# Performance work log

Measured on AMD Instinct MI355X. Metric: run time of the kernel, lower is better.

The kernel has to match this reference:

```python
import jax, jax.numpy as jnp
import numpy as np

B, T, C = 4, 2048, 1024
N_HEAD = 16
HEAD_DIM = C // N_HEAD

def setup_inputs() -> dict:
    key = jax.random.key(0)
    k1, k2, k3 = jax.random.split(key, 3)
    x = jax.random.normal(k1, (B, T, C), dtype=jnp.float32)
    # nn.Linear(C, 3C, bias=False): weight [3C, C], y = x @ W.T
    w_qkv = jax.random.normal(k2, (3 * C, C), dtype=jnp.float32) * (1.0 / np.sqrt(C))
    w_proj = jax.random.normal(k3, (C, C), dtype=jnp.float32) * (1.0 / np.sqrt(C))
    return {"x": x, "w_qkv": w_qkv, "w_proj": w_proj}

def reference(x, w_qkv, w_proj):
    Bx, Tx, Cx = x.shape
    qkv = x @ w_qkv.T  # [B,T,3C]
    q, k, v = jnp.split(qkv, 3, axis=-1)
    def heads(t):
        return t.reshape(Bx, Tx, N_HEAD, HEAD_DIM).transpose(0, 2, 1, 3)  # [B,H,T,D]
    q, k, v = heads(q), heads(k), heads(v)
    scale = HEAD_DIM ** -0.5
    att = jnp.einsum('bhtd,bhsd->bhts', q, k) * scale  # [B,H,T,T]
    causal = jnp.tril(jnp.ones((Tx, Tx), dtype=bool))
    att = jnp.where(causal[None, None], att, -jnp.inf)
    att = jax.nn.softmax(att, axis=-1)
    y = jnp.einsum('bhts,bhsd->bhtd', att, v)  # [B,H,T,D]
    y = y.transpose(0, 2, 1, 3).reshape(Bx, Tx, Cx)
    return y @ w_proj.T
```

## Files before the change

kernel.cpp:

```cpp
#include <hip/hip_runtime.h>
#include <hip/hip_bf16.h>

typedef __attribute__((ext_vector_type(8))) short bf16x8;
typedef __attribute__((ext_vector_type(4))) float f32x4;
typedef __attribute__((ext_vector_type(4))) unsigned short ushort4v;
typedef __attribute__((ext_vector_type(2))) unsigned uint2v;

__device__ __forceinline__ unsigned short f2bf(float f) {
  union { float f; unsigned u; } v; v.f = f;
  unsigned r = v.u + 0x7FFFu + ((v.u >> 16) & 1u);
  return (unsigned short)(r >> 16);
}

__device__ __forceinline__ unsigned pack_bf2(float lo, float hi) {
  __hip_bfloat162 h = __float22bfloat162_rn(make_float2(lo, hi));
  union { __hip_bfloat162 h; unsigned u; } cv; cv.h = h; return cv.u;
}

__device__ __forceinline__ void gll16(const void* g, void* l) {
  __builtin_amdgcn_global_load_lds((const __attribute__((address_space(1))) void*)g,
                                   (__attribute__((address_space(3))) void*)l, 16, 0, 0);
}

#define MFMA16(a, b, c) __builtin_amdgcn_mfma_f32_16x16x32_bf16((a), (b), (c), 0, 0, 0)

__global__ void cvt_f32_bf16(const float* __restrict__ s, unsigned short* __restrict__ d, int n) {
  int i = (blockIdx.x * blockDim.x + threadIdx.x) * 4;
  if (i >= n) return;
  float4 f = *(const float4*)(s + i);
  ushort4v r;
  r[0] = f2bf(f.x); r[1] = f2bf(f.y); r[2] = f2bf(f.z); r[3] = f2bf(f.w);
  *(ushort4v*)(d + i) = r;
}

template<int EPI, int MIF>
__global__ __launch_bounds__(512, 1)
void gemm4p(const unsigned short* __restrict__ A,
            const unsigned short* __restrict__ B,
            unsigned short* __restrict__ obf,
            float* __restrict__ of32,
            int M, int N, int K) {
  extern __shared__ unsigned short lds[];
  constexpr int BM = MIF * 32;
  constexpr int ABUF = BM * 32;
  constexpr int BBASE = 3 * ABUF;
  const int tid = threadIdx.x, wid = tid >> 6, lane = tid & 63;
  const int c = lane & 15, g = lane >> 4;
  const int wm = wid >> 2, wn = wid & 3;
  const int nbn = N >> 8;
  const int nwg = gridDim.x;
  int wg = (blockIdx.x & 7) * (nwg >> 3) + (blockIdx.x >> 3);
  const int m0 = (wg / nbn) * BM, n0 = (wg % nbn) * 256;
  const int NT = K >> 5;
  const size_t rb = (size_t)K * 2;
  const int swz = (c & 3) << 4;

  const int r16 = lane >> 2;
  const int sl = (lane & 3) ^ (r16 & 3);
  const char* Ag = (const char*)A + (size_t)(m0 + r16) * rb + sl * 16;
  const char* Bg = (const char*)B + (size_t)(n0 + r16) * rb + sl * 16;

  auto stageA = [&](int t, int buf) {
#pragma unroll
    for (int j = 0; j < MIF / 4; ++j) {
      int ch = wid * (MIF / 4) + j;
      gll16(Ag + (size_t)(ch * 16) * rb + t * 64, lds + buf * ABUF + ch * 512);
    }
  };
  auto stageB = [&](int t, int buf) {
#pragma unroll
    for (int j = 0; j < 2; ++j) {
      int ch = wid * 2 + j;
      gll16(Bg + (size_t)(ch * 16) * rb + t * 64, lds + BBASE + buf * 8192 + ch * 512);
    }
  };

  f32x4 acc[MIF][4];
#pragma unroll
  for (int i = 0; i < MIF; ++i)
#pragma unroll
    for (int j = 0; j < 4; ++j) acc[i][j] = f32x4{0.f, 0.f, 0.f, 0.f};

  stageA(0, 0); stageB(0, 0); stageA(1, 1); stageB(1, 1);
  if constexpr (MIF == 8) { asm volatile("s_waitcnt vmcnt(4)" ::: "memory"); }
  else                    { asm volatile("s_waitcnt vmcnt(3)" ::: "memory"); }
  __builtin_amdgcn_s_barrier();

  for (int t = 0; t < NT; ++t) {
    const int cur = t % 3;
    const unsigned short* Ac = lds + cur * ABUF;
    const unsigned short* Bc = lds + BBASE + cur * 8192;
    const bool more = (t + 2 < NT);
    const int nbuf = (t + 2) % 3;
    bf16x8 af[MIF], bfr[4];
#pragma unroll
    for (int mi = 0; mi < MIF / 2; ++mi) {
      int arow = wm * (MIF * 16) + mi * 16 + c;
      af[mi] = *(const bf16x8*)((const char*)Ac + arow * 64 + ((g * 16) ^ swz));
    }
#pragma unroll
    for (int ni = 0; ni < 4; ++ni) {
      int brow = wn * 64 + ni * 16 + c;
      bfr[ni] = *(const bf16x8*)((const char*)Bc + brow * 64 + ((g * 16) ^ swz));
    }
    if (more) stageA(t + 2, nbuf);
    __builtin_amdgcn_s_barrier();
    asm volatile("s_waitcnt lgkmcnt(0)" ::: "memory");
    __builtin_amdgcn_sched_barrier(0);
    __builtin_amdgcn_s_setprio(1);
#pragma unroll
    for (int mi = 0; mi < MIF / 2; ++mi)
#pragma unroll
      for (int ni = 0; ni < 4; ++ni)
        acc[mi][ni] = MFMA16(af[mi], bfr[ni], acc[mi][ni]);
    __builtin_amdgcn_s_setprio(0);
    __builtin_amdgcn_s_barrier();
#pragma unroll
    for (int mi = MIF / 2; mi < MIF; ++mi) {
      int arow = wm * (MIF * 16) + mi * 16 + c;
      af[mi] = *(const bf16x8*)((const char*)Ac + arow * 64 + ((g * 16) ^ swz));
    }
    if (more) stageB(t + 2, nbuf);
    __builtin_amdgcn_s_barrier();
    asm volatile("s_waitcnt lgkmcnt(0)" ::: "memory");
    __builtin_amdgcn_sched_barrier(0);
    __builtin_amdgcn_s_setprio(1);
#pragma unroll
    for (int mi = MIF / 2; mi < MIF; ++mi)
#pragma unroll
      for (int ni = 0; ni < 4; ++ni)
        acc[mi][ni] = MFMA16(af[mi], bfr[ni], acc[mi][ni]);
    __builtin_amdgcn_s_setprio(0);
    if (more) {
      if constexpr (MIF == 8) { asm volatile("s_waitcnt vmcnt(4)" ::: "memory"); }
      else                    { asm volatile("s_waitcnt vmcnt(3)" ::: "memory"); }
    } else {
      asm volatile("s_waitcnt vmcnt(0)" ::: "memory");
    }
    __builtin_amdgcn_s_barrier();
  }

#pragma unroll
  for (int mi = 0; mi < MIF; ++mi)
#pragma unroll
    for (int ni = 0; ni < 4; ++ni)
#pragma unroll
      for (int r4 = 0; r4 < 4; ++r4) {
        float v = acc[mi][ni][r4];
        int mg = m0 + wm * (MIF * 16) + mi * 16 + g * 4 + r4;
        int ng = n0 + wn * 64 + ni * 16 + c;
        if (EPI == 0) {
          int which = ng >> 10, rem = ng & 1023;
          int hh = rem >> 6, dd = rem & 63;
          int bb = mg >> 11, tt = mg & 2047;
          size_t idx = (size_t)which * 8388608u + ((size_t)(bb * 16 + hh) * 2048 + tt) * 64 + dd;
          obf[idx] = f2bf(v);
        } else {
          of32[(size_t)mg * N + ng] = v;
        }
      }
}

__global__ __launch_bounds__(256, 6)
void attn_fwd(const unsigned short* __restrict__ qb,
              const unsigned short* __restrict__ kb,
              const unsigned short* __restrict__ vb,
              unsigned short* __restrict__ yb) {
  __shared__ unsigned short Kt[64 * 64];
  __shared__ unsigned short Vt[64 * 64];
  __shared__ unsigned short Pl[4 * 16 * 72];
  const int tid = threadIdx.x, w = tid >> 6, lane = tid & 63;
  const int c = lane & 15, g = lane >> 4;
  const int bh = blockIdx.x & 63;
  const int qt = 31 - (blockIdx.x >> 6);
  const int q0 = qt * 64;
  const int b = bh >> 4, h = bh & 15;
  const size_t hb = (size_t)bh * 131072;
  const float GAM = 0.125f * 1.44269504089f;

  const unsigned short* qp = qb + hb + (size_t)(q0 + w * 16 + c) * 64;
  bf16x8 qf0 = *(const bf16x8*)(qp + g * 8);
  bf16x8 qf1 = *(const bf16x8*)(qp + 32 + g * 8);

  f32x4 yacc[4];
#pragma unroll
  for (int i = 0; i < 4; ++i) yacc[i] = f32x4{0.f, 0.f, 0.f, 0.f};
  float mrun = -1e30f, lsum = 0.f;
  unsigned short* pw = Pl + w * (16 * 72);

  for (int kv = 0; kv <= qt; ++kv) {
    const int kv0 = kv * 64;
    const bool diag = (kv == qt);
    if (kv) __syncthreads();
#pragma unroll
    for (int r = 0; r < 2; ++r) {
      int chunk = w * 2 + r;
      int row = chunk * 8 + (lane >> 3);
      int bo = (lane & 7) * 16;
      int sbo = bo ^ ((row & 7) << 4);
      gll16((const char*)(kb + hb + (size_t)(kv0 + row) * 64) + sbo, Kt + chunk * 512);
    }
    {
      int kv2 = (lane & 31) * 2;
      int dblk = w * 16 + (lane >> 5) * 8;
      const unsigned short* vp = vb + hb + (size_t)(kv0 + kv2) * 64 + dblk;
      bf16x8 r0 = *(const bf16x8*)(vp);
      bf16x8 r1 = *(const bf16x8*)(vp + 64);
#pragma unroll
      for (int i = 0; i < 8; ++i) {
        int d = dblk + i;
        unsigned pk2 = ((unsigned)(unsigned short)r0[i]) | (((unsigned)(unsigned short)r1[i]) << 16);
        *(unsigned*)(Vt + d * 64 + (kv2 ^ ((d & 7) << 3))) = pk2;
      }
    }
    __syncthreads();

    f32x4 sacc[4];
#pragma unroll
    for (int nt = 0; nt < 4; ++nt) sacc[nt] = f32x4{0.f, 0.f, 0.f, 0.f};
#pragma unroll
    for (int kk = 0; kk < 2; ++kk)
#pragma unroll
      for (int nt = 0; nt < 4; ++nt) {
        int row = nt * 16 + c;
        bf16x8 kf = *(const bf16x8*)(Kt + row * 64 + ((kk * 32 + g * 8) ^ ((row & 7) << 3)));
        sacc[nt] = MFMA16(kf, (kk ? qf1 : qf0), sacc[nt]);
      }

    if (diag) {
      int ql = w * 16 + c;
#pragma unroll
      for (int nt = 0; nt < 4; ++nt)
#pragma unroll
        for (int r = 0; r < 4; ++r)
          if (nt * 16 + g * 4 + r > ql) sacc[nt][r] = -1e30f;
    }

    float m0 = -1e30f;
#pragma unroll
    for (int nt = 0; nt < 4; ++nt) {
      float a = fmaxf(fmaxf(sacc[nt][0], sacc[nt][1]), fmaxf(sacc[nt][2], sacc[nt][3]));
      m0 = fmaxf(m0, a);
    }
    m0 = fmaxf(m0, __shfl_xor(m0, 16));
    m0 = fmaxf(m0, __shfl_xor(m0, 32));

    if (__any(m0 > mrun + 32.0f)) {
      float mnew = fmaxf(mrun, m0);
      float corr = __builtin_amdgcn_exp2f(GAM * (mrun - mnew));
      lsum *= corr;
#pragma unroll
      for (int dt = 0; dt < 4; ++dt) yacc[dt] *= corr;
      mrun = mnew;
    }

    float bexp = -GAM * mrun;
    float psum = 0.f;
#pragma unroll
    for (int nt = 0; nt < 4; ++nt) {
      float p0 = __builtin_amdgcn_exp2f(fmaf(sacc[nt][0], GAM, bexp));
      float p1 = __builtin_amdgcn_exp2f(fmaf(sacc[nt][1], GAM, bexp));
      float p2 = __builtin_amdgcn_exp2f(fmaf(sacc[nt][2], GAM, bexp));
      float p3 = __builtin_amdgcn_exp2f(fmaf(sacc[nt][3], GAM, bexp));
      psum += (p0 + p1) + (p2 + p3);
      uint2v pkv;
      pkv[0] = pack_bf2(p0, p1);
      pkv[1] = pack_bf2(p2, p3);
      *(uint2v*)(pw + c * 72 + nt * 16 + g * 4) = pkv;
    }
    lsum += psum;

#pragma unroll
    for (int kk = 0; kk < 2; ++kk) {
      bf16x8 pb = *(const bf16x8*)(pw + c * 72 + kk * 32 + g * 8);
#pragma unroll
      for (int dt = 0; dt < 4; ++dt) {
        int n = dt * 16 + c;
        bf16x8 vf = *(const bf16x8*)(Vt + n * 64 + ((kk * 32 + g * 8) ^ ((n & 7) << 3)));
        yacc[dt] = MFMA16(vf, pb, yacc[dt]);
      }
    }
  }

  lsum += __shfl_xor(lsum, 16);
  lsum += __shfl_xor(lsum, 32);
  float inv = 1.0f / lsum;
  int row = q0 + w * 16 + c;
  unsigned short* yp = yb + ((size_t)(b * 2048 + row)) * 1024 + h * 64;
#pragma unroll
  for (int dt = 0; dt < 4; ++dt) {
    uint2v pkv;
    pkv[0] = pack_bf2(yacc[dt][0] * inv, yacc[dt][1] * inv);
    pkv[1] = pack_bf2(yacc[dt][2] * inv, yacc[dt][3] * inv);
    *(uint2v*)(yp + dt * 16 + g * 4) = pkv;
  }
}

extern "C" void kernel_launch(void* const* d_in, const int* in_sizes, int n_in,
                              void* d_out, int out_size, void* d_ws, size_t ws_size,
                              hipStream_t stream) {
  const float* x     = (const float*)d_in[0];
  const float* wqkv  = (const float*)d_in[1];
  const float* wproj = (const float*)d_in[2];
  float* out = (float*)d_out;

  unsigned short* ws     = (unsigned short*)d_ws;
  unsigned short* xb     = ws;
  unsigned short* wqkvb  = xb + 8388608;
  unsigned short* wprojb = wqkvb + 3145728;
  unsigned short* qkvb   = wprojb + 1048576;
  unsigned short* yb     = qkvb + 3 * 8388608;

  cvt_f32_bf16<<<8192, 256, 0, stream>>>(x, xb, 8388608);
  cvt_f32_bf16<<<3072, 256, 0, stream>>>(wqkv, wqkvb, 3145728);
  cvt_f32_bf16<<<1024, 256, 0, stream>>>(wproj, wprojb, 1048576);

  gemm4p<0, 8><<<384, 512, 98304, stream>>>(xb, wqkvb, qkvb, nullptr, 8192, 3072, 1024);
  attn_fwd<<<2048, 256, 0, stream>>>(qkvb, qkvb + 8388608, qkvb + 2 * 8388608, yb);
  gemm4p<1, 4><<<256, 512, 73728, stream>>>(yb, wprojb, nullptr, out, 8192, 1024, 1024);
}
```

Baseline: 185.3 us.

## Merge conversion kernels and restructure GEMMs into 256-thread two-per-CU tiles with vectorized epilogue

Result: faster. 172.8 us (-6.7%).

```diff
diff --git a/kernel.cpp b/kernel.cpp
--- a/kernel.cpp
+++ b/kernel.cpp
@@ -24,54 +24,57 @@
 
 #define MFMA16(a, b, c) __builtin_amdgcn_mfma_f32_16x16x32_bf16((a), (b), (c), 0, 0, 0)
 
-__global__ void cvt_f32_bf16(const float* __restrict__ s, unsigned short* __restrict__ d, int n) {
+__global__ void cvt3(const float* __restrict__ x, const float* __restrict__ wq,
+                     const float* __restrict__ wp,
+                     unsigned short* __restrict__ xb, unsigned short* __restrict__ wqb,
+                     unsigned short* __restrict__ wpb) {
   int i = (blockIdx.x * blockDim.x + threadIdx.x) * 4;
-  if (i >= n) return;
-  float4 f = *(const float4*)(s + i);
+  const float* s; unsigned short* d;
+  if (i < 8388608)        { s = x  + i;                 d = xb  + i; }
+  else if (i < 11534336)  { s = wq + (i - 8388608);     d = wqb + (i - 8388608); }
+  else                    { s = wp + (i - 11534336);    d = wpb + (i - 11534336); }
+  float4 f = *(const float4*)s;
   ushort4v r;
   r[0] = f2bf(f.x); r[1] = f2bf(f.y); r[2] = f2bf(f.z); r[3] = f2bf(f.w);
-  *(ushort4v*)(d + i) = r;
+  *(ushort4v*)d = r;
 }
 
 template<int EPI, int MIF>
-__global__ __launch_bounds__(512, 1)
-void gemm4p(const unsigned short* __restrict__ A,
-            const unsigned short* __restrict__ B,
-            unsigned short* __restrict__ obf,
-            float* __restrict__ of32,
-            int M, int N, int K) {
-  extern __shared__ unsigned short lds[];
+__global__ __launch_bounds__(256, 2)
+void gemmf(const unsigned short* __restrict__ A,
+           const unsigned short* __restrict__ B,
+           unsigned short* __restrict__ obf,
+           float* __restrict__ of32,
+           int M, int N, int K) {
+  extern __shared__ char lds[];
   constexpr int BM = MIF * 32;
-  constexpr int ABUF = BM * 32;
-  constexpr int BBASE = 3 * ABUF;
+  constexpr int BUFB = (BM + 128) * 64;
   const int tid = threadIdx.x, wid = tid >> 6, lane = tid & 63;
   const int c = lane & 15, g = lane >> 4;
-  const int wm = wid >> 2, wn = wid & 3;
-  const int nbn = N >> 8;
-  const int nwg = gridDim.x;
-  int wg = (blockIdx.x & 7) * (nwg >> 3) + (blockIdx.x >> 3);
-  const int m0 = (wg / nbn) * BM, n0 = (wg % nbn) * 256;
+  const int wm = wid >> 1, wn = wid & 1;
+  const int nbn = N >> 7;
+  const int wg = (blockIdx.x & 7) * (gridDim.x >> 3) + (blockIdx.x >> 3);
+  const int m0 = (wg / nbn) * BM, n0 = (wg % nbn) * 128;
   const int NT = K >> 5;
   const size_t rb = (size_t)K * 2;
-  const int swz = (c & 3) << 4;
-
-  const int r16 = lane >> 2;
-  const int sl = (lane & 3) ^ (r16 & 3);
-  const char* Ag = (const char*)A + (size_t)(m0 + r16) * rb + sl * 16;
-  const char* Bg = (const char*)B + (size_t)(n0 + r16) * rb + sl * 16;
-
-  auto stageA = [&](int t, int buf) {
-#pragma unroll
-    for (int j = 0; j < MIF / 4; ++j) {
-      int ch = wid * (MIF / 4) + j;
-      gll16(Ag + (size_t)(ch * 16) * rb + t * 64, lds + buf * ABUF + ch * 512);
-    }
-  };
-  auto stageB = [&](int t, int buf) {
+  const int rk = (c ^ (c >> 2)) & 3;
+
+  const int lrow = lane >> 2;
+  const int lslot = (lane & 3) ^ (((lane >> 2) ^ (lane >> 4)) & 3);
+  const char* Ab = (const char*)A + (size_t)m0 * rb + (size_t)lrow * rb + lslot * 16;
+  const char* Bb = (const char*)B + (size_t)n0 * rb + (size_t)lrow * rb + lslot * 16;
+
+  auto stage = [&](int t, int buf) {
+    char* base = lds + buf * BUFB;
+#pragma unroll
+    for (int j = 0; j < MIF / 2; ++j) {
+      int ch = wid * (MIF / 2) + j;
+      gll16(Ab + (size_t)(ch * 16) * rb + t * 64, base + ch * 1024);
+    }
 #pragma unroll
     for (int j = 0; j < 2; ++j) {
       int ch = wid * 2 + j;
-      gll16(Bg + (size_t)(ch * 16) * rb + t * 64, lds + BBASE + buf * 8192 + ch * 512);
+      gll16(Bb + (size_t)(ch * 16) * rb + t * 64, base + BM * 64 + ch * 1024);
     }
   };
 
@@ -81,59 +84,39 @@
 #pragma unroll
     for (int j = 0; j < 4; ++j) acc[i][j] = f32x4{0.f, 0.f, 0.f, 0.f};
 
-  stageA(0, 0); stageB(0, 0); stageA(1, 1); stageB(1, 1);
-  if constexpr (MIF == 8) { asm volatile("s_waitcnt vmcnt(4)" ::: "memory"); }
-  else                    { asm volatile("s_waitcnt vmcnt(3)" ::: "memory"); }
+  stage(0, 0); stage(1, 1);
+  if constexpr (MIF == 8) { asm volatile("s_waitcnt vmcnt(6)" ::: "memory"); }
+  else                    { asm volatile("s_waitcnt vmcnt(4)" ::: "memory"); }
   __builtin_amdgcn_s_barrier();
 
+  const int col = ((g ^ rk) << 4);
   for (int t = 0; t < NT; ++t) {
-    const int cur = t % 3;
-    const unsigned short* Ac = lds + cur * ABUF;
-    const unsigned short* Bc = lds + BBASE + cur * 8192;
-    const bool more = (t + 2 < NT);
-    const int nbuf = (t + 2) % 3;
+    const char* base = lds + (t % 3) * BUFB;
     bf16x8 af[MIF], bfr[4];
 #pragma unroll
-    for (int mi = 0; mi < MIF / 2; ++mi) {
+    for (int mi = 0; mi < MIF; ++mi) {
       int arow = wm * (MIF * 16) + mi * 16 + c;
-      af[mi] = *(const bf16x8*)((const char*)Ac + arow * 64 + ((g * 16) ^ swz));
+      af[mi] = *(const bf16x8*)(base + arow * 64 + col);
     }
 #pragma unroll
     for (int ni = 0; ni < 4; ++ni) {
       int brow = wn * 64 + ni * 16 + c;
-      bfr[ni] = *(const bf16x8*)((const char*)Bc + brow * 64 + ((g * 16) ^ swz));
-    }
-    if (more) stageA(t + 2, nbuf);
-    __builtin_amdgcn_s_barrier();
+      bfr[ni] = *(const bf16x8*)(base + BM * 64 + brow * 64 + col);
+    }
+    const bool more = (t + 2 < NT);
+    if (more) stage(t + 2, (t + 2) % 3);
     asm volatile("s_waitcnt lgkmcnt(0)" ::: "memory");
     __builtin_amdgcn_sched_barrier(0);
     __builtin_amdgcn_s_setprio(1);
 #pragma unroll
-    for (int mi = 0; mi < MIF / 2; ++mi)
+    for (int mi = 0; mi < MIF; ++mi)
 #pragma unroll
       for (int ni = 0; ni < 4; ++ni)
-        acc[mi][ni] = MFMA16(af[mi], bfr[ni], acc[mi][ni]);
-    __builtin_amdgcn_s_setprio(0);
-    __builtin_amdgcn_s_barrier();
-#pragma unroll
-    for (int mi = MIF / 2; mi < MIF; ++mi) {
-      int arow = wm * (MIF * 16) + mi * 16 + c;
-      af[mi] = *(const bf16x8*)((const char*)Ac + arow * 64 + ((g * 16) ^ swz));
-    }
-    if (more) stageB(t + 2, nbuf);
-    __builtin_amdgcn_s_barrier();
-    asm volatile("s_waitcnt lgkmcnt(0)" ::: "memory");
-    __builtin_amdgcn_sched_barrier(0);
-    __builtin_amdgcn_s_setprio(1);
-#pragma unroll
-    for (int mi = MIF / 2; mi < MIF; ++mi)
-#pragma unroll
-      for (int ni = 0; ni < 4; ++ni)
-        acc[mi][ni] = MFMA16(af[mi], bfr[ni], acc[mi][ni]);
+        acc[mi][ni] = MFMA16(bfr[ni], af[mi], acc[mi][ni]);
     __builtin_amdgcn_s_setprio(0);
     if (more) {
-      if constexpr (MIF == 8) { asm volatile("s_waitcnt vmcnt(4)" ::: "memory"); }
-      else                    { asm volatile("s_waitcnt vmcnt(3)" ::: "memory"); }
+      if constexpr (MIF == 8) { asm volatile("s_waitcnt vmcnt(6)" ::: "memory"); }
+      else                    { asm volatile("s_waitcnt vmcnt(4)" ::: "memory"); }
     } else {
       asm volatile("s_waitcnt vmcnt(0)" ::: "memory");
     }
@@ -141,24 +124,28 @@
   }
 
 #pragma unroll
-  for (int mi = 0; mi < MIF; ++mi)
-#pragma unroll
-    for (int ni = 0; ni < 4; ++ni)
-#pragma unroll
-      for (int r4 = 0; r4 < 4; ++r4) {
-        float v = acc[mi][ni][r4];
-        int mg = m0 + wm * (MIF * 16) + mi * 16 + g * 4 + r4;
-        int ng = n0 + wn * 64 + ni * 16 + c;
-        if (EPI == 0) {
-          int which = ng >> 10, rem = ng & 1023;
-          int hh = rem >> 6, dd = rem & 63;
-          int bb = mg >> 11, tt = mg & 2047;
-          size_t idx = (size_t)which * 8388608u + ((size_t)(bb * 16 + hh) * 2048 + tt) * 64 + dd;
-          obf[idx] = f2bf(v);
-        } else {
-          of32[(size_t)mg * N + ng] = v;
-        }
+  for (int mi = 0; mi < MIF; ++mi) {
+    int mg = m0 + wm * (MIF * 16) + mi * 16 + c;
+    if (EPI == 0) {
+      int bb = mg >> 11, tt = mg & 2047;
+      size_t rowbase = ((size_t)(bb * 16) * 2048 + tt) * 64;
+#pragma unroll
+      for (int ni = 0; ni < 4; ++ni) {
+        int ng = n0 + wn * 64 + ni * 16 + g * 4;
+        int which = ng >> 10, rem = ng & 1023;
+        int hh = rem >> 6, dd = rem & 63;
+        uint2v pk;
+        pk[0] = pack_bf2(acc[mi][ni][0], acc[mi][ni][1]);
+        pk[1] = pack_bf2(acc[mi][ni][2], acc[mi][ni][3]);
+        *(uint2v*)(obf + (size_t)which * 8388608u + rowbase + (size_t)hh * 131072 + dd) = pk;
       }
+    } else {
+      float* orow = of32 + (size_t)mg * N + n0 + wn * 64 + g * 4;
+#pragma unroll
+      for (int ni = 0; ni < 4; ++ni)
+        *(f32x4*)(orow + ni * 16) = acc[mi][ni];
+    }
+  }
 }
 
 __global__ __launch_bounds__(256, 6)
@@ -311,11 +298,9 @@
   unsigned short* qkvb   = wprojb + 1048576;
   unsigned short* yb     = qkvb + 3 * 8388608;
 
-  cvt_f32_bf16<<<8192, 256, 0, stream>>>(x, xb, 8388608);
-  cvt_f32_bf16<<<3072, 256, 0, stream>>>(wqkv, wqkvb, 3145728);
-  cvt_f32_bf16<<<1024, 256, 0, stream>>>(wproj, wprojb, 1048576);
-
-  gemm4p<0, 8><<<384, 512, 98304, stream>>>(xb, wqkvb, qkvb, nullptr, 8192, 3072, 1024);
+  cvt3<<<12288, 256, 0, stream>>>(x, wqkv, wproj, xb, wqkvb, wprojb);
+
+  gemmf<0, 8><<<768, 256, 73728, stream>>>(xb, wqkvb, qkvb, nullptr, 8192, 3072, 1024);
   attn_fwd<<<2048, 256, 0, stream>>>(qkvb, qkvb + 8388608, qkvb + 2 * 8388608, yb);
-  gemm4p<1, 4><<<256, 512, 73728, stream>>>(yb, wprojb, nullptr, out, 8192, 1024, 1024);
-}
+  gemmf<1, 4><<<512, 256, 49152, stream>>>(yb, wprojb, nullptr, out, 8192, 1024, 1024);
+}
```
